# Optimization experiments

Hardware: AMD Instinct MI355X
Metric: run time of the kernel (lower is better)

## Reference

```python
import jax, jax.numpy as jnp
import numpy as np

B, T, D = 32, 1024, 1024
N, L = 256, 768
H = 16
TE = 2048


def layernorm(x, g, b, eps=1e-5):
    m = jnp.mean(x, axis=-1, keepdims=True)
    v = jnp.var(x, axis=-1, keepdims=True)
    return (x - m) * jax.lax.rsqrt(v + eps) * g + b


def setup_inputs() -> dict:
    key = jax.random.key(0)
    ks = jax.random.split(key, 16)
    s = 0.02
    return {
        "x": jax.random.normal(ks[0], (B, T, D), jnp.float32),
        "xf": jax.random.normal(ks[1], (B, N, L), jnp.float32),
        "emb": jax.random.normal(ks[2], (B, TE), jnp.float32),
        "src_mask": jnp.ones((B, T, 1), jnp.float32),
        "cond_type": jax.random.randint(ks[3], (B, 1, 1), 0, 100),
        # LayerNorm params
        "ln_x_g": jnp.ones((D,), jnp.float32), "ln_x_b": jnp.zeros((D,), jnp.float32),
        "ln_t_g": jnp.ones((L,), jnp.float32), "ln_t_b": jnp.zeros((L,), jnp.float32),
        # Q/K/V projections
        "Wq": jax.random.normal(ks[4], (D, D), jnp.float32) * s, "bq": jnp.zeros((D,), jnp.float32),
        "Wk": jax.random.normal(ks[5], (L, D), jnp.float32) * s, "bk": jnp.zeros((D,), jnp.float32),
        "Wv": jax.random.normal(ks[6], (L, D), jnp.float32) * s, "bv": jnp.zeros((D,), jnp.float32),
        # StylizationBlock: SiLU -> Linear(TE, 2D); LayerNorm(D); SiLU -> Linear(D, D)
        "We": jax.random.normal(ks[7], (TE, 2 * D), jnp.float32) * s, "be": jnp.zeros((2 * D,), jnp.float32),
        "ln_y_g": jnp.ones((D,), jnp.float32), "ln_y_b": jnp.zeros((D,), jnp.float32),
        "Wo": jax.random.normal(ks[8], (D, D), jnp.float32) * s, "bo": jnp.zeros((D,), jnp.float32),
    }


def reference(x, xf, emb, src_mask, cond_type,
              ln_x_g, ln_x_b, ln_t_g, ln_t_b,
              Wq, bq, Wk, bk, Wv, bv,
              We, be, ln_y_g, ln_y_b, Wo, bo):
    Bh, Th, Dh = x.shape
    Nn = xf.shape[1]
    head = Dh // H

    # text condition gate: (B,1,1), constant per batch element
    tcond = (cond_type % 10 > 0).astype(x.dtype).reshape(Bh, 1, 1)

    q = (layernorm(x, ln_x_g, ln_x_b) @ Wq + bq).reshape(Bh, Th, H, head)
    xf_n = layernorm(xf, ln_t_g, ln_t_b)
    k = (xf_n @ Wk + bk).reshape(Bh, Nn, H, head)

    # B,T,N,H scores (note: no 1/sqrt(d) scaling, as in the original)
    att = jnp.einsum('bthd,bnhd->btnh', q, k)
    att = att + (1.0 - tcond.reshape(Bh, 1, 1, 1)) * -1000000.0
    att = jax.nn.softmax(att, axis=2)

    v = ((xf_n @ Wv + bv) * tcond).reshape(Bh, Nn, H, head)
    y = jnp.einsum('btnh,bnhd->bthd', att, v).reshape(Bh, Th, Dh)

    # StylizationBlock (dropout inactive in eval)
    emb_out = jax.nn.silu(emb) @ We + be            # B, 2D
    scale, shift = jnp.split(emb_out, 2, axis=-1)   # B, D each
    h = layernorm(y, ln_y_g, ln_y_b) * (1.0 + scale[:, None, :]) + shift[:, None, :]
    h = jax.nn.silu(h) @ Wo + bo
    return x + h
```

## Files before the change

kernel.cpp:

```cpp
#include <hip/hip_runtime.h>
#include <hip/hip_bf16.h>

#define DEV __device__ __forceinline__

typedef __attribute__((ext_vector_type(8))) short bf16x8;
typedef __attribute__((ext_vector_type(4))) float f32x4;
typedef __attribute__((ext_vector_type(8))) unsigned short u16x8;

DEV unsigned short f2bf(float f){
  unsigned int b = __float_as_uint(f);
  return (unsigned short)((b + 0x7fffu + ((b >> 16) & 1u)) >> 16);
}
DEV float bf2f(unsigned short u){ return __uint_as_float(((unsigned int)u)<<16); }

DEV float silu_f(float v){ return v / (1.f + __expf(-v)); }

DEV void gl_lds16(const void* g, void* l){
  __builtin_amdgcn_global_load_lds((const __attribute__((address_space(1))) void*)g,
                                   (__attribute__((address_space(3))) void*)l, 16, 0, 0);
}

__global__ __launch_bounds__(256) void ln_rows(const float* __restrict__ x,
    const float* __restrict__ g, const float* __restrict__ bt,
    unsigned short* __restrict__ out, int D, int nvec)
{
  int row = blockIdx.x, t = threadIdx.x;
  const float4* xr = (const float4*)(x + (size_t)row * D);
  float4 v = make_float4(0.f,0.f,0.f,0.f);
  if (t < nvec) v = xr[t];
  float s  = v.x+v.y+v.z+v.w;
  float s2 = v.x*v.x+v.y*v.y+v.z*v.z+v.w*v.w;
  #pragma unroll
  for (int o=32;o;o>>=1){ s += __shfl_down(s,o,64); s2 += __shfl_down(s2,o,64); }
  __shared__ float red[8];
  if ((t&63)==0){ red[t>>6]=s; red[4+(t>>6)]=s2; }
  __syncthreads();
  float fs  = red[0]+red[1]+red[2]+red[3];
  float fs2 = red[4]+red[5]+red[6]+red[7];
  float mean = fs / (float)D;
  float var  = fmaxf(fs2/(float)D - mean*mean, 0.f);
  float rstd = rsqrtf(var + 1e-5f);
  if (t < nvec){
    float4 gv = ((const float4*)g)[t];
    float4 bv = ((const float4*)bt)[t];
    ushort4 o4;
    o4.x = f2bf((v.x-mean)*rstd*gv.x + bv.x);
    o4.y = f2bf((v.y-mean)*rstd*gv.y + bv.y);
    o4.z = f2bf((v.z-mean)*rstd*gv.z + bv.z);
    o4.w = f2bf((v.w-mean)*rstd*gv.w + bv.w);
    *(ushort4*)(out + (size_t)row*D + t*4) = o4;
  }
}

__global__ __launch_bounds__(256) void wconv(const float* __restrict__ W,
    unsigned short* __restrict__ Wt, int K, int N)
{
  __shared__ float tile[32][33];
  int n0 = blockIdx.x<<5, k0 = blockIdx.y<<5;
  int tx = threadIdx.x & 31, ty = threadIdx.x >> 5;
  #pragma unroll
  for (int i=0;i<4;i++)
    tile[ty + i*8][tx] = W[(size_t)(k0 + ty + i*8)*N + n0 + tx];
  __syncthreads();
  #pragma unroll
  for (int i=0;i<4;i++)
    Wt[(size_t)(n0 + ty + i*8)*K + k0 + tx] = f2bf(tile[tx][ty + i*8]);
}

__global__ __launch_bounds__(256) void bcat(const float* __restrict__ a,
    const float* __restrict__ b, float* __restrict__ o)
{
  int i = blockIdx.x*256 + threadIdx.x;
  o[i] = (i < 1024) ? a[i] : b[i-1024];
}

template<int EPI>
__global__ __launch_bounds__(256,2) void gemm128(
  const unsigned char* __restrict__ A, const unsigned char* __restrict__ Wt,
  const float* __restrict__ bias, void* __restrict__ Cout,
  const float* __restrict__ Xadd, int M, int N, int K, int gxshift)
{
  __shared__ __align__(16) unsigned char lds[65536];
  const int nwg = gridDim.x;
  const int chunk = nwg >> 3;
  const int wg = blockIdx.x;
  const int lg = (wg & 7) * chunk + (wg >> 3);
  const int bx = lg & ((1<<gxshift)-1);
  const int by = lg >> gxshift;
  const int tid = threadIdx.x, w = tid>>6, lane = tid&63;
  const int l15 = lane&15, lq = lane>>4;
  const int m0 = by<<7, n0 = bx<<7;
  const size_t K2 = (size_t)K<<1;
  const int KT = K>>6;
  const int wr = (w>>1)&1, wc = w&1;
  const int srow = lane>>3;
  const int scb  = (lane&7)<<4;

  f32x4 acc[4][4];
  f32x4 zero = {0.f,0.f,0.f,0.f};
  #pragma unroll
  for (int i=0;i<4;i++)
    #pragma unroll
    for (int j=0;j<4;j++) acc[i][j] = zero;

  auto stage = [&](int buf, int kt){
    unsigned char* ldsA = lds + buf*32768;
    const size_t kb = (size_t)kt<<7;
    #pragma unroll
    for (int inst=0; inst<4; ++inst){
      int base = w*1024 + inst*4096;
      int row  = (base>>7) + srow;
      int cs   = scb ^ ((row&7)<<4);
      gl_lds16(A  + (size_t)(m0+row)*K2 + kb + cs, ldsA + base);
      gl_lds16(Wt + (size_t)(n0+row)*K2 + kb + cs, ldsA + 16384 + base);
    }
  };

  stage(0, 0);
  __syncthreads();
  for (int kt=0; kt<KT; ++kt){
    if (kt+1 < KT) stage((kt+1)&1, kt+1);
    const unsigned char* ldsA = lds + (kt&1)*32768;
    const unsigned char* ldsB = ldsA + 16384;
    bf16x8 af[2][4], bfr[2][4];
    #pragma unroll
    for (int i=0;i<4;i++){
      int r = wr*64 + i*16 + l15;
      int rb = r<<7, sw = (r&7)<<4;
      af[0][i] = *(const bf16x8*)(ldsA + rb + ((lq*16) ^ sw));
      af[1][i] = *(const bf16x8*)(ldsA + rb + ((64 + lq*16) ^ sw));
    }
    #pragma unroll
    for (int j=0;j<4;j++){
      int r = wc*64 + j*16 + l15;
      int rb = r<<7, sw = (r&7)<<4;
      bfr[0][j] = *(const bf16x8*)(ldsB + rb + ((lq*16) ^ sw));
      bfr[1][j] = *(const bf16x8*)(ldsB + rb + ((64 + lq*16) ^ sw));
    }
    #pragma unroll
    for (int kc=0;kc<2;kc++)
      #pragma unroll
      for (int i=0;i<4;i++)
        #pragma unroll
        for (int j=0;j<4;j++)
          acc[i][j] = __builtin_amdgcn_mfma_f32_16x16x32_bf16(af[kc][i], bfr[kc][j], acc[i][j], 0,0,0);
    __syncthreads();
  }
  #pragma unroll
  for (int j=0;j<4;j++){
    int n = n0 + wc*64 + j*16 + l15;
    float bv = bias[n];
    #pragma unroll
    for (int i=0;i<4;i++){
      int mb = m0 + wr*64 + i*16 + lq*4;
      #pragma unroll
      for (int r=0;r<4;r++){
        size_t idx = (size_t)(mb+r)*N + n;
        float val = acc[i][j][r] + bv;
        if (EPI==0) ((unsigned short*)Cout)[idx] = f2bf(val);
        else        ((float*)Cout)[idx] = Xadd[idx] + val;
      }
    }
  }
}

__global__ __launch_bounds__(256) void vtransp(const unsigned short* __restrict__ v,
                                               int vstride, unsigned char* __restrict__ vt)
{
  __shared__ __align__(16) unsigned short tile[16384];
  int h = blockIdx.x, b = blockIdx.y, tid = threadIdx.x;
  const unsigned short* src = v + (size_t)b*256*vstride + h*64;
  #pragma unroll
  for (int it=0; it<8; ++it){
    int idx = it*256 + tid;
    int n = idx>>3, dc = idx&7;
    *(f32x4*)&tile[n*64 + dc*8] = *(const f32x4*)(src + (size_t)n*vstride + dc*8);
  }
  __syncthreads();
  unsigned char* dst = vt + (size_t)(b*16+h)*32768;
  #pragma unroll
  for (int it=0; it<8; ++it){
    int idx = it*256 + tid;
    int d = idx>>5, nc = idx&31;
    u16x8 o;
    #pragma unroll
    for (int j=0;j<8;j++) o[j] = tile[(nc*8+j)*64 + d];
    *(u16x8*)(dst + d*512 + ((nc*16) ^ ((d&7)<<4))) = o;
  }
}

__global__ __launch_bounds__(256,2) void attn64(
  const unsigned char* __restrict__ qg, const unsigned char* __restrict__ kg,
  int kstride, const unsigned char* __restrict__ vtg, const int* __restrict__ cond,
  unsigned short* __restrict__ yout)
{
  __shared__ __align__(16) unsigned char lds[73728];
  const int wg = blockIdx.x;
  const int lg = (wg & 7) * 1024 + (wg >> 3);
  const int t0 = (lg & 15) * 64;
  const int h  = (lg >> 4) & 15;
  const int b  = lg >> 8;
  const int tid = threadIdx.x, w = tid>>6, lane = tid&63;
  const int l15 = lane&15, lq = lane>>4;

  const unsigned char* kbase = kg + (size_t)b*256*kstride + (size_t)h*128;
  const unsigned char* vtb   = vtg + (size_t)(b*16+h)*32768;
  #pragma unroll
  for (int i=0;i<8;i++){
    int base = (w*8+i)*1024;
    int n  = (base>>7) + (lane>>3);
    int cb = (lane&7)<<4;
    gl_lds16(kbase + (size_t)n*kstride + (cb ^ ((n&7)<<4)), lds + base);
    gl_lds16(vtb + base + lane*16, lds + 32768 + base);
  }
  const unsigned char* qbase = qg + (size_t)(b*1024 + t0)*2048 + h*128;
  #pragma unroll
  for (int i=0;i<2;i++){
    int row = i*32 + (tid>>3);
    int cs  = ((tid&7)<<4) ^ ((row&7)<<4);
    gl_lds16(qbase + (size_t)row*2048 + cs, lds + 65536 + i*4096 + w*1024);
  }
  __syncthreads();

  const int qr = w*16 + l15;
  const int qsw = (qr&7)<<4;
  bf16x8 aq0 = *(const bf16x8*)(lds + 65536 + qr*128 + ((lq*16) ^ qsw));
  bf16x8 aq1 = *(const bf16x8*)(lds + 65536 + qr*128 + ((64 + lq*16) ^ qsw));

  f32x4 zero = {0.f,0.f,0.f,0.f};
  f32x4 s[16];
  #pragma unroll
  for (int nt=0;nt<16;nt++) s[nt] = zero;
  #pragma unroll
  for (int nt=0;nt<16;nt++){
    int n = nt*16 + l15;
    int rb = n<<7, sw = (n&7)<<4;
    bf16x8 kb0 = *(const bf16x8*)(lds + rb + ((lq*16) ^ sw));
    bf16x8 kb1 = *(const bf16x8*)(lds + rb + ((64 + lq*16) ^ sw));
    s[nt] = __builtin_amdgcn_mfma_f32_16x16x32_bf16(aq0, kb0, s[nt], 0,0,0);
    s[nt] = __builtin_amdgcn_mfma_f32_16x16x32_bf16(aq1, kb1, s[nt], 0,0,0);
  }
  #pragma unroll
  for (int r=0;r<4;r++){
    float m = s[0][r];
    #pragma unroll
    for (int nt=1;nt<16;nt++) m = fmaxf(m, s[nt][r]);
    m = fmaxf(m, __shfl_xor(m,1,64));
    m = fmaxf(m, __shfl_xor(m,2,64));
    m = fmaxf(m, __shfl_xor(m,4,64));
    m = fmaxf(m, __shfl_xor(m,8,64));
    float sum = 0.f;
    #pragma unroll
    for (int nt=0;nt<16;nt++){ float p = __expf(s[nt][r]-m); s[nt][r]=p; sum+=p; }
    sum += __shfl_xor(sum,1,64);
    sum += __shfl_xor(sum,2,64);
    sum += __shfl_xor(sum,4,64);
    sum += __shfl_xor(sum,8,64);
    float inv = 1.f/sum;
    #pragma unroll
    for (int nt=0;nt<16;nt++) s[nt][r] *= inv;
  }
  __syncthreads();
  #pragma unroll
  for (int nt=0;nt<16;nt++){
    int n = nt*16 + l15;
    int nb = (n>>3)<<4, nr = (n&7)<<1;
    #pragma unroll
    for (int r=0;r<4;r++){
      int tl = w*16 + lq*4 + r;
      *(unsigned short*)(lds + tl*512 + ((nb ^ ((tl&7)<<4)) | nr)) = f2bf(s[nt][r]);
    }
  }
  __syncthreads();
  f32x4 yv[4];
  #pragma unroll
  for (int dt=0;dt<4;dt++) yv[dt] = zero;
  const int tl = w*16 + l15;
  const int swp = (tl&7)<<4;
  #pragma unroll
  for (int kc=0;kc<8;kc++){
    bf16x8 pa = *(const bf16x8*)(lds + tl*512 + ((kc*64 + lq*16) ^ swp));
    #pragma unroll
    for (int dt=0;dt<4;dt++){
      int d = dt*16 + l15;
      bf16x8 vbv = *(const bf16x8*)(lds + 32768 + d*512 + ((kc*64 + lq*16) ^ ((d&7)<<4)));
      yv[dt] = __builtin_amdgcn_mfma_f32_16x16x32_bf16(pa, vbv, yv[dt], 0,0,0);
    }
  }
  float tc = (cond[b] % 10 > 0) ? 1.f : 0.f;
  #pragma unroll
  for (int dt=0;dt<4;dt++){
    #pragma unroll
    for (int r=0;r<4;r++){
      int tt = t0 + w*16 + lq*4 + r;
      yout[(size_t)(b*1024 + tt)*1024 + h*64 + dt*16 + l15] = f2bf(yv[dt][r]*tc);
    }
  }
}

__global__ __launch_bounds__(256) void embgemm(const float* __restrict__ emb,
    const float* __restrict__ We, float* __restrict__ epart)
{
  __shared__ float a[32][128];
  int cb = blockIdx.x, ks = blockIdx.y, tid = threadIdx.x;
  int k0 = ks<<7;
  #pragma unroll
  for (int it=0; it<4; ++it){
    int fi = it*256 + tid;
    int r = fi>>5, c4 = (fi&31)<<2;
    float4 vv = *(const float4*)(emb + (size_t)r*2048 + k0 + c4);
    vv.x = silu_f(vv.x); vv.y = silu_f(vv.y); vv.z = silu_f(vv.z); vv.w = silu_f(vv.w);
    *(float4*)&a[r][c4] = vv;
  }
  __syncthreads();
  int c0 = (cb<<8) + tid;
  float acc[32];
  #pragma unroll
  for (int r=0;r<32;r++) acc[r]=0.f;
  for (int kk=0;kk<128;kk++){
    float wv = We[(size_t)(k0+kk)*2048 + c0];
    #pragma unroll
    for (int r=0;r<32;r++) acc[r] += a[r][kk]*wv;
  }
  #pragma unroll
  for (int r=0;r<32;r++) epart[(size_t)(ks*32 + r)*2048 + c0] = acc[r];
}

__global__ __launch_bounds__(256) void embred(const float* __restrict__ epart,
    const float* __restrict__ be, float* __restrict__ eo)
{
  int idx = blockIdx.x*256 + threadIdx.x;
  float s = be[idx & 2047];
  #pragma unroll
  for (int ks=0;ks<16;ks++) s += epart[(size_t)ks*65536 + idx];
  eo[idx] = s;
}

__global__ __launch_bounds__(256) void styl(const unsigned short* __restrict__ y,
    const float* __restrict__ g, const float* __restrict__ bt,
    const float* __restrict__ eo, unsigned short* __restrict__ hout)
{
  int row = blockIdx.x, t = threadIdx.x, b = row>>10;
  ushort4 yv4 = ((const ushort4*)(y + (size_t)row*1024))[t];
  float in[4] = {bf2f(yv4.x), bf2f(yv4.y), bf2f(yv4.z), bf2f(yv4.w)};
  float s  = in[0]+in[1]+in[2]+in[3];
  float s2 = in[0]*in[0]+in[1]*in[1]+in[2]*in[2]+in[3]*in[3];
  #pragma unroll
  for (int o=32;o;o>>=1){ s += __shfl_down(s,o,64); s2 += __shfl_down(s2,o,64); }
  __shared__ float red[8];
  if ((t&63)==0){ red[t>>6]=s; red[4+(t>>6)]=s2; }
  __syncthreads();
  float fs  = red[0]+red[1]+red[2]+red[3];
  float fs2 = red[4]+red[5]+red[6]+red[7];
  float mean = fs*(1.f/1024.f);
  float var  = fmaxf(fs2*(1.f/1024.f) - mean*mean, 0.f);
  float rstd = rsqrtf(var + 1e-5f);
  float4 gv = ((const float4*)g)[t];
  float4 bv = ((const float4*)bt)[t];
  float4 sc = ((const float4*)(eo + (size_t)b*2048))[t];
  float4 sh = ((const float4*)(eo + (size_t)b*2048 + 1024))[t];
  float gg[4]  = {gv.x,gv.y,gv.z,gv.w};
  float bb[4]  = {bv.x,bv.y,bv.z,bv.w};
  float scs[4] = {sc.x,sc.y,sc.z,sc.w};
  float shs[4] = {sh.x,sh.y,sh.z,sh.w};
  unsigned short oo[4];
  #pragma unroll
  for (int c=0;c<4;c++){
    float hv = (in[c]-mean)*rstd*gg[c] + bb[c];
    hv = hv*(1.f+scs[c]) + shs[c];
    oo[c] = f2bf(silu_f(hv));
  }
  ushort4 o4; o4.x=oo[0]; o4.y=oo[1]; o4.z=oo[2]; o4.w=oo[3];
  *(ushort4*)(hout + (size_t)row*1024 + t*4) = o4;
}

extern "C" void kernel_launch(void* const* d_in, const int* in_sizes, int n_in,
                              void* d_out, int out_size, void* d_ws, size_t ws_size,
                              hipStream_t stream) {
  const float* x      = (const float*)d_in[0];
  const float* xf     = (const float*)d_in[1];
  const float* emb    = (const float*)d_in[2];
  const int*   cond   = (const int*)d_in[4];
  const float* ln_x_g = (const float*)d_in[5];
  const float* ln_x_b = (const float*)d_in[6];
  const float* ln_t_g = (const float*)d_in[7];
  const float* ln_t_b = (const float*)d_in[8];
  const float* Wq     = (const float*)d_in[9];
  const float* bq     = (const float*)d_in[10];
  const float* Wk     = (const float*)d_in[11];
  const float* bk     = (const float*)d_in[12];
  const float* Wv     = (const float*)d_in[13];
  const float* bv     = (const float*)d_in[14];
  const float* We     = (const float*)d_in[15];
  const float* be     = (const float*)d_in[16];
  const float* ln_y_g = (const float*)d_in[17];
  const float* ln_y_b = (const float*)d_in[18];
  const float* Wo     = (const float*)d_in[19];
  const float* bo     = (const float*)d_in[20];
  float* out = (float*)d_out;

  unsigned char* ws = (unsigned char*)d_ws;
  size_t off = 0;
  auto take = [&](size_t n){ unsigned char* p = ws + off; off += (n + 255) & ~(size_t)255; return p; };
  unsigned char* r1   = take(67108864);
  unsigned char* qb   = take(67108864);
  unsigned char* xfn  = take(12582912);
  unsigned char* kvb  = take(33554432);
  unsigned char* vtb  = take(16777216);
  unsigned char* wqt  = take(2097152);
  unsigned char* wkvt = take(3145728);
  unsigned char* wot  = take(2097152);
  unsigned char* eo   = take(262144);
  unsigned char* bkv  = take(8192);
  float* epart = (float*)r1;

  dim3 blk(256);
  wconv<<<dim3(32,32), blk, 0, stream>>>(Wq, (unsigned short*)wqt, 1024, 1024);
  wconv<<<dim3(32,24), blk, 0, stream>>>(Wk, (unsigned short*)wkvt,  768, 1024);
  wconv<<<dim3(32,24), blk, 0, stream>>>(Wv, (unsigned short*)wkvt + (size_t)1024*768, 768, 1024);
  wconv<<<dim3(32,32), blk, 0, stream>>>(Wo, (unsigned short*)wot, 1024, 1024);
  bcat<<<8, blk, 0, stream>>>(bk, bv, (float*)bkv);
  ln_rows<<<32768, blk, 0, stream>>>(x,  ln_x_g, ln_x_b, (unsigned short*)r1,  1024, 256);
  ln_rows<<<8192,  blk, 0, stream>>>(xf, ln_t_g, ln_t_b, (unsigned short*)xfn,  768, 192);
  gemm128<0><<<2048, blk, 0, stream>>>(r1,  wqt,  bq, qb, nullptr, 32768, 1024, 1024, 3);
  gemm128<0><<<1024, blk, 0, stream>>>(xfn, wkvt, (const float*)bkv, kvb, nullptr, 8192, 2048, 768, 4);
  vtransp<<<dim3(16,32), blk, 0, stream>>>((const unsigned short*)kvb + 1024, 2048, vtb);
  embgemm<<<dim3(8,16), blk, 0, stream>>>(emb, We, epart);
  embred<<<256, blk, 0, stream>>>(epart, be, (float*)eo);
  attn64<<<8192, blk, 0, stream>>>(qb, kvb, 4096, vtb, cond, (unsigned short*)qb);
  styl<<<32768, blk, 0, stream>>>((const unsigned short*)qb, ln_y_g, ln_y_b, (const float*)eo, (unsigned short*)r1);
  gemm128<1><<<2048, blk, 0, stream>>>(r1, wot, bo, out, x, 32768, 1024, 1024, 3);
}
```

Measured before the change: 486.4 us.

## Merge prep kernels into one launch and fuse V transpose into KV GEMM epilogue

Combines the four weight-conversion launches, the bias concat and both LayerNorm launches into a single kernel that dispatches on block index. The KV projection GEMM gains an epilogue mode that writes K to its own buffer and scatters V directly into the swizzled transposed layout that attention reads, which removes the separate transpose kernel and its round trip through memory. The aim is fewer launches and less memory traffic. The trade-off is that the V scatter writes 2-byte elements, which coalesce poorly in the epilogue.

```diff
diff --git a/kernel.cpp b/kernel.cpp
--- a/kernel.cpp
+++ b/kernel.cpp
@@ -20,14 +20,56 @@
                                    (__attribute__((address_space(3))) void*)l, 16, 0, 0);
 }
 
-__global__ __launch_bounds__(256) void ln_rows(const float* __restrict__ x,
-    const float* __restrict__ g, const float* __restrict__ bt,
-    unsigned short* __restrict__ out, int D, int nvec)
+DEV void wtile(const float* W, unsigned short* Wt, int K, int N, int nt, int kt, int tid,
+               float (*tile)[33])
+{
+  int n0 = nt<<5, k0 = kt<<5;
+  int tx = tid & 31, ty = tid >> 5;
+  #pragma unroll
+  for (int i=0;i<4;i++)
+    tile[ty + i*8][tx] = W[(size_t)(k0 + ty + i*8)*N + n0 + tx];
+  __syncthreads();
+  #pragma unroll
+  for (int i=0;i<4;i++)
+    Wt[(size_t)(n0 + ty + i*8)*K + k0 + tx] = f2bf(tile[tx][ty + i*8]);
+}
+
+__global__ __launch_bounds__(256) void prep_ln(
+    const float* __restrict__ x, const float* __restrict__ xf,
+    const float* __restrict__ gx, const float* __restrict__ bx_,
+    const float* __restrict__ gt, const float* __restrict__ bt,
+    unsigned short* __restrict__ ox, unsigned short* __restrict__ ot,
+    const float* __restrict__ Wq, const float* __restrict__ Wk,
+    const float* __restrict__ Wv, const float* __restrict__ Wo,
+    const float* __restrict__ bk, const float* __restrict__ bv,
+    unsigned short* __restrict__ wqt, unsigned short* __restrict__ wkvt,
+    unsigned short* __restrict__ wot, float* __restrict__ bkv)
 {
   int row = blockIdx.x, t = threadIdx.x;
-  const float4* xr = (const float4*)(x + (size_t)row * D);
+  if (row >= 40960){
+    __shared__ float tile[32][33];
+    int id = row - 40960;
+    if (id < 8){
+      int i = id*256 + t;
+      bkv[i] = (i < 1024) ? bk[i] : bv[i-1024];
+      return;
+    }
+    id -= 8;
+    if (id < 1024){ wtile(Wq, wqt, 1024, 1024, id & 31, id >> 5, t, tile); return; }
+    id -= 1024;
+    if (id < 768){ wtile(Wk, wkvt, 768, 1024, id & 31, id >> 5, t, tile); return; }
+    id -= 768;
+    if (id < 768){ wtile(Wv, wkvt + (size_t)1024*768, 768, 1024, id & 31, id >> 5, t, tile); return; }
+    id -= 768;
+    wtile(Wo, wot, 1024, 1024, id & 31, id >> 5, t, tile);
+    return;
+  }
+  const float* src; const float* g; const float* bb; unsigned short* out;
+  int D, nvec;
+  if (row < 32768){ src = x + (size_t)row*1024; g = gx; bb = bx_; out = ox + (size_t)row*1024; D = 1024; nvec = 256; }
+  else { int r2 = row - 32768; src = xf + (size_t)r2*768; g = gt; bb = bt; out = ot + (size_t)r2*768; D = 768; nvec = 192; }
   float4 v = make_float4(0.f,0.f,0.f,0.f);
-  if (t < nvec) v = xr[t];
+  if (t < nvec) v = ((const float4*)src)[t];
   float s  = v.x+v.y+v.z+v.w;
   float s2 = v.x*v.x+v.y*v.y+v.z*v.z+v.w*v.w;
   #pragma unroll
@@ -42,43 +84,22 @@
   float rstd = rsqrtf(var + 1e-5f);
   if (t < nvec){
     float4 gv = ((const float4*)g)[t];
-    float4 bv = ((const float4*)bt)[t];
+    float4 bv4 = ((const float4*)bb)[t];
     ushort4 o4;
-    o4.x = f2bf((v.x-mean)*rstd*gv.x + bv.x);
-    o4.y = f2bf((v.y-mean)*rstd*gv.y + bv.y);
-    o4.z = f2bf((v.z-mean)*rstd*gv.z + bv.z);
-    o4.w = f2bf((v.w-mean)*rstd*gv.w + bv.w);
-    *(ushort4*)(out + (size_t)row*D + t*4) = o4;
-  }
-}
-
-__global__ __launch_bounds__(256) void wconv(const float* __restrict__ W,
-    unsigned short* __restrict__ Wt, int K, int N)
-{
-  __shared__ float tile[32][33];
-  int n0 = blockIdx.x<<5, k0 = blockIdx.y<<5;
-  int tx = threadIdx.x & 31, ty = threadIdx.x >> 5;
-  #pragma unroll
-  for (int i=0;i<4;i++)
-    tile[ty + i*8][tx] = W[(size_t)(k0 + ty + i*8)*N + n0 + tx];
-  __syncthreads();
-  #pragma unroll
-  for (int i=0;i<4;i++)
-    Wt[(size_t)(n0 + ty + i*8)*K + k0 + tx] = f2bf(tile[tx][ty + i*8]);
-}
-
-__global__ __launch_bounds__(256) void bcat(const float* __restrict__ a,
-    const float* __restrict__ b, float* __restrict__ o)
-{
-  int i = blockIdx.x*256 + threadIdx.x;
-  o[i] = (i < 1024) ? a[i] : b[i-1024];
+    o4.x = f2bf((v.x-mean)*rstd*gv.x + bv4.x);
+    o4.y = f2bf((v.y-mean)*rstd*gv.y + bv4.y);
+    o4.z = f2bf((v.z-mean)*rstd*gv.z + bv4.z);
+    o4.w = f2bf((v.w-mean)*rstd*gv.w + bv4.w);
+    *(ushort4*)(out + t*4) = o4;
+  }
 }
 
 template<int EPI>
 __global__ __launch_bounds__(256,2) void gemm128(
   const unsigned char* __restrict__ A, const unsigned char* __restrict__ Wt,
   const float* __restrict__ bias, void* __restrict__ Cout,
-  const float* __restrict__ Xadd, int M, int N, int K, int gxshift)
+  const float* __restrict__ Xadd, unsigned char* __restrict__ vt,
+  int M, int N, int K, int gxshift)
 {
   __shared__ __align__(16) unsigned char lds[65536];
   const int nwg = gridDim.x;
@@ -149,43 +170,32 @@
   #pragma unroll
   for (int j=0;j<4;j++){
     int n = n0 + wc*64 + j*16 + l15;
-    float bv = bias[n];
+    float bvs = bias[n];
     #pragma unroll
     for (int i=0;i<4;i++){
       int mb = m0 + wr*64 + i*16 + lq*4;
       #pragma unroll
       for (int r=0;r<4;r++){
-        size_t idx = (size_t)(mb+r)*N + n;
-        float val = acc[i][j][r] + bv;
-        if (EPI==0) ((unsigned short*)Cout)[idx] = f2bf(val);
-        else        ((float*)Cout)[idx] = Xadd[idx] + val;
+        int m = mb + r;
+        float val = acc[i][j][r] + bvs;
+        if (EPI==0){
+          ((unsigned short*)Cout)[(size_t)m*N + n] = f2bf(val);
+        } else if (EPI==1){
+          size_t idx = (size_t)m*N + n;
+          ((float*)Cout)[idx] = Xadd[idx] + val;
+        } else {
+          if (n0 < 1024){
+            ((unsigned short*)Cout)[(size_t)m*1024 + n] = f2bf(val);
+          } else {
+            int d  = (n-1024)&63;
+            int hh = (n-1024)>>6;
+            int bb_ = m>>8, nk = m&255;
+            *(unsigned short*)(vt + ((size_t)(bb_*16+hh)<<15) + d*512
+                + (((nk>>3)<<4) ^ ((d&7)<<4)) + ((nk&7)<<1)) = f2bf(val);
+          }
+        }
       }
     }
-  }
-}
-
-__global__ __launch_bounds__(256) void vtransp(const unsigned short* __restrict__ v,
-                                               int vstride, unsigned char* __restrict__ vt)
-{
-  __shared__ __align__(16) unsigned short tile[16384];
-  int h = blockIdx.x, b = blockIdx.y, tid = threadIdx.x;
-  const unsigned short* src = v + (size_t)b*256*vstride + h*64;
-  #pragma unroll
-  for (int it=0; it<8; ++it){
-    int idx = it*256 + tid;
-    int n = idx>>3, dc = idx&7;
-    *(f32x4*)&tile[n*64 + dc*8] = *(const f32x4*)(src + (size_t)n*vstride + dc*8);
-  }
-  __syncthreads();
-  unsigned char* dst = vt + (size_t)(b*16+h)*32768;
-  #pragma unroll
-  for (int it=0; it<8; ++it){
-    int idx = it*256 + tid;
-    int d = idx>>5, nc = idx&31;
-    u16x8 o;
-    #pragma unroll
-    for (int j=0;j<8;j++) o[j] = tile[(nc*8+j)*64 + d];
-    *(u16x8*)(dst + d*512 + ((nc*16) ^ ((d&7)<<4))) = o;
   }
 }
 
@@ -405,7 +415,7 @@
   unsigned char* r1   = take(67108864);
   unsigned char* qb   = take(67108864);
   unsigned char* xfn  = take(12582912);
-  unsigned char* kvb  = take(33554432);
+  unsigned char* kb   = take(16777216);
   unsigned char* vtb  = take(16777216);
   unsigned char* wqt  = take(2097152);
   unsigned char* wkvt = take(3145728);
@@ -415,19 +425,15 @@
   float* epart = (float*)r1;
 
   dim3 blk(256);
-  wconv<<<dim3(32,32), blk, 0, stream>>>(Wq, (unsigned short*)wqt, 1024, 1024);
-  wconv<<<dim3(32,24), blk, 0, stream>>>(Wk, (unsigned short*)wkvt,  768, 1024);
-  wconv<<<dim3(32,24), blk, 0, stream>>>(Wv, (unsigned short*)wkvt + (size_t)1024*768, 768, 1024);
-  wconv<<<dim3(32,32), blk, 0, stream>>>(Wo, (unsigned short*)wot, 1024, 1024);
-  bcat<<<8, blk, 0, stream>>>(bk, bv, (float*)bkv);
-  ln_rows<<<32768, blk, 0, stream>>>(x,  ln_x_g, ln_x_b, (unsigned short*)r1,  1024, 256);
-  ln_rows<<<8192,  blk, 0, stream>>>(xf, ln_t_g, ln_t_b, (unsigned short*)xfn,  768, 192);
-  gemm128<0><<<2048, blk, 0, stream>>>(r1,  wqt,  bq, qb, nullptr, 32768, 1024, 1024, 3);
-  gemm128<0><<<1024, blk, 0, stream>>>(xfn, wkvt, (const float*)bkv, kvb, nullptr, 8192, 2048, 768, 4);
-  vtransp<<<dim3(16,32), blk, 0, stream>>>((const unsigned short*)kvb + 1024, 2048, vtb);
+  prep_ln<<<44552, blk, 0, stream>>>(x, xf, ln_x_g, ln_x_b, ln_t_g, ln_t_b,
+      (unsigned short*)r1, (unsigned short*)xfn,
+      Wq, Wk, Wv, Wo, bk, bv,
+      (unsigned short*)wqt, (unsigned short*)wkvt, (unsigned short*)wot, (float*)bkv);
+  gemm128<0><<<2048, blk, 0, stream>>>(r1, wqt, bq, qb, nullptr, nullptr, 32768, 1024, 1024, 3);
+  gemm128<2><<<1024, blk, 0, stream>>>(xfn, wkvt, (const float*)bkv, kb, nullptr, vtb, 8192, 2048, 768, 4);
   embgemm<<<dim3(8,16), blk, 0, stream>>>(emb, We, epart);
   embred<<<256, blk, 0, stream>>>(epart, be, (float*)eo);
-  attn64<<<8192, blk, 0, stream>>>(qb, kvb, 4096, vtb, cond, (unsigned short*)qb);
+  attn64<<<8192, blk, 0, stream>>>(qb, kb, 2048, vtb, cond, (unsigned short*)qb);
   styl<<<32768, blk, 0, stream>>>((const unsigned short*)qb, ln_y_g, ln_y_b, (const float*)eo, (unsigned short*)r1);
-  gemm128<1><<<2048, blk, 0, stream>>>(r1, wot, bo, out, x, 32768, 1024, 1024, 3);
-}
+  gemm128<1><<<2048, blk, 0, stream>>>(r1, wot, bo, out, x, nullptr, 32768, 1024, 1024, 3);
+}
```

Measured after the change: 462.4 us. 1.05x faster.
